# Kernel optimization log

Hardware: AMD Instinct MI355X
Metric: run time of the kernel (lower is better)

## Reference

```python
import jax, jax.numpy as jnp
import numpy as np

INPUT_DIM = 128
DEPTH = 6
HIDDEN = 64
NUM_INNER = 2 ** DEPTH - 1  # 63
NUM_LEAVES = 2 ** DEPTH     # 64


def setup_inputs() -> dict:
    key = jax.random.key(0)
    ks = jax.random.split(key, 6)
    x = jax.random.normal(ks[0], (65536, INPUT_DIM), dtype=jnp.float32)
    s1 = 1.0 / np.sqrt(INPUT_DIM)
    s2 = 1.0 / np.sqrt(HIDDEN)
    W1 = jax.random.uniform(ks[1], (NUM_INNER, INPUT_DIM, HIDDEN), minval=-s1, maxval=s1, dtype=jnp.float32)
    b1 = jax.random.uniform(ks[2], (NUM_INNER, HIDDEN), minval=-s1, maxval=s1, dtype=jnp.float32)
    W2 = jax.random.uniform(ks[3], (NUM_INNER, HIDDEN), minval=-s2, maxval=s2, dtype=jnp.float32)
    b2 = jax.random.uniform(ks[4], (NUM_INNER,), minval=-s2, maxval=s2, dtype=jnp.float32)
    leaf = jax.random.normal(ks[5], (NUM_LEAVES, 1), dtype=jnp.float32)
    return {"x": x, "W1": W1, "b1": b1, "W2": W2, "b2": b2, "leaf": leaf}


def reference(x, W1, b1, W2, b2, leaf):
    # All inner-node MLPs as one batched GEMM pair: [B, N] node probabilities
    h = jax.nn.relu(jnp.einsum('bi,nih->bnh', x, W1) + b1)      # [B, N, H]
    probs = jax.nn.sigmoid(jnp.einsum('bnh,nh->bn', h, W2) + b2)  # [B, N]

    # Original code walks node_idx = 2*node_idx+1 unconditionally, so the chain
    # of used node indices is 2^k - 1 for k = 0..depth-1.
    chain = jnp.array([2 ** k - 1 for k in range(DEPTH)], dtype=jnp.int32)
    p_chain = probs[:, chain]  # [B, D]

    # Bit k (LSB first) of leaf index selects p (bit=1) vs 1-p (bit=0)
    leaves = np.arange(NUM_LEAVES)
    bits = jnp.asarray(((leaves[:, None] >> np.arange(DEPTH)[None, :]) & 1).astype(np.float32))  # [L, D]

    # path_probs[b, l] = prod_k ( bits[l,k]*p + (1-bits[l,k])*(1-p) )
    factors = bits[None, :, :] * p_chain[:, None, :] + (1.0 - bits[None, :, :]) * (1.0 - p_chain[:, None, :])  # [B, L, D]
    path_probs = jnp.prod(factors, axis=-1)  # [B, L]

    return (path_probs @ leaf)[:, 0]  # [B]
```

## Files before the change

kernel.cpp:

```cpp
#include <hip/hip_runtime.h>

typedef __attribute__((ext_vector_type(4))) float f32x4;
typedef __attribute__((ext_vector_type(8))) short bf16x8;
typedef __attribute__((ext_vector_type(4))) unsigned int u32x4;

#define IDIM    128
#define HID     64
#define TDEPTH  6
#define MTILE   64
#define NWAVES  6
#define BLOCK   (NWAVES * 64)
#define T_TILES 4

__device__ __forceinline__ unsigned short f2bf(float f) {
    unsigned int u = __builtin_bit_cast(unsigned int, f);
    unsigned int r = (u + 0x7FFFu + ((u >> 16) & 1u)) >> 16;
    return (unsigned short)r;
}

__device__ __forceinline__ unsigned int f2bf_pk(float f0, float f1) {
    unsigned int u0 = __builtin_bit_cast(unsigned int, f0);
    unsigned int u1 = __builtin_bit_cast(unsigned int, f1);
    unsigned int t0 = u0 + 0x7FFFu + ((u0 >> 16) & 1u);
    unsigned int t1 = u1 + 0x7FFFu + ((u1 >> 16) & 1u);
    return (t1 & 0xFFFF0000u) | (t0 >> 16);
}

__global__ __launch_bounds__(BLOCK, 2)
void sdt_kernel(const float* __restrict__ x, const float* __restrict__ W1,
                const float* __restrict__ b1, const float* __restrict__ W2,
                const float* __restrict__ b2, const float* __restrict__ leaf,
                float* __restrict__ out) {
    __shared__ unsigned short xs[2][MTILE][IDIM + 8];
    __shared__ float p_lds[TDEPTH][MTILE];
    __shared__ float pp[4][MTILE];

    const int tid   = threadIdx.x;
    const int tile0 = blockIdx.x * T_TILES;

    const int wave = tid >> 6;
    const int lane = tid & 63;
    const int node = (1 << wave) - 1;
    const int lcol = lane & 15;
    const int lq   = lane >> 4;

    const float4* xv = reinterpret_cast<const float4*>(x);

    float4 sreg[6];
    {
        const float4* xt = xv + (size_t)tile0 * (MTILE * IDIM / 4);
        #pragma unroll
        for (int i = 0; i < 5; i++) sreg[i] = xt[tid + i * BLOCK];
        if (tid < 128) sreg[5] = xt[5 * BLOCK + tid];
    }

    bf16x8 bfrag[4][4];
    {
        const float* wsrc = W1 + (size_t)node * IDIM * HID + lcol;
        #pragma unroll
        for (int ks = 0; ks < 4; ks++) {
            const int k0 = ks * 32 + lq * 8;
            #pragma unroll
            for (int ct = 0; ct < 4; ct++) {
                const float* wc = wsrc + (size_t)k0 * HID + ct * 16;
                u32x4 pk;
                #pragma unroll
                for (int jp = 0; jp < 4; jp++)
                    pk[jp] = f2bf_pk(wc[(2 * jp) * HID], wc[(2 * jp + 1) * HID]);
                bfrag[ks][ct] = __builtin_bit_cast(bf16x8, pk);
            }
        }
    }

    float b1v[4], w2v[4];
    #pragma unroll
    for (int ct = 0; ct < 4; ct++) {
        int col = ct * 16 + lcol;
        b1v[ct] = b1[node * HID + col];
        w2v[ct] = W2[node * HID + col];
    }
    const float bias2 = b2[node];

    #pragma unroll
    for (int i = 0; i < 5; i++) {
        int f = tid + i * BLOCK, row = f >> 5, c4 = f & 31;
        float4 v = sreg[i];
        unsigned long long pk =
            (unsigned long long)f2bf(v.x) |
            ((unsigned long long)f2bf(v.y) << 16) |
            ((unsigned long long)f2bf(v.z) << 32) |
            ((unsigned long long)f2bf(v.w) << 48);
        *reinterpret_cast<unsigned long long*>(&xs[0][row][c4 * 4]) = pk;
    }
    if (tid < 128) {
        int f = 5 * BLOCK + tid, row = f >> 5, c4 = f & 31;
        float4 v = sreg[5];
        unsigned long long pk =
            (unsigned long long)f2bf(v.x) |
            ((unsigned long long)f2bf(v.y) << 16) |
            ((unsigned long long)f2bf(v.z) << 32) |
            ((unsigned long long)f2bf(v.w) << 48);
        *reinterpret_cast<unsigned long long*>(&xs[0][row][c4 * 4]) = pk;
    }
    __syncthreads();

    int cur = 0;
    for (int t = 0; t < T_TILES; ++t) {
        const bool pf = (t + 1 < T_TILES);
        if (pf) {
            const float4* xt = xv + (size_t)(tile0 + t + 1) * (MTILE * IDIM / 4);
            #pragma unroll
            for (int i = 0; i < 5; i++) sreg[i] = xt[tid + i * BLOCK];
            if (tid < 128) sreg[5] = xt[5 * BLOCK + tid];
        }

        f32x4 acc[4][4];
        #pragma unroll
        for (int rt = 0; rt < 4; rt++)
            #pragma unroll
            for (int ct = 0; ct < 4; ct++)
                acc[rt][ct] = (f32x4){0.f, 0.f, 0.f, 0.f};
        #pragma unroll
        for (int ks = 0; ks < 4; ks++) {
            bf16x8 afrag[4];
            #pragma unroll
            for (int rt = 0; rt < 4; rt++)
                afrag[rt] = *reinterpret_cast<const bf16x8*>(
                    &xs[cur][rt * 16 + lcol][ks * 32 + lq * 8]);
            #pragma unroll
            for (int rt = 0; rt < 4; rt++)
                #pragma unroll
                for (int ct = 0; ct < 4; ct++)
                    acc[rt][ct] = __builtin_amdgcn_mfma_f32_16x16x32_bf16(
                        afrag[rt], bfrag[ks][ct], acc[rt][ct], 0, 0, 0);
        }

        #pragma unroll
        for (int rt = 0; rt < 4; rt++) {
            #pragma unroll
            for (int r = 0; r < 4; r++) {
                float s = 0.f;
                #pragma unroll
                for (int ct = 0; ct < 4; ct++) {
                    float v = acc[rt][ct][r] + b1v[ct];
                    v = v > 0.f ? v : 0.f;
                    s += v * w2v[ct];
                }
                #pragma unroll
                for (int d = 1; d < 16; d <<= 1)
                    s += __shfl_xor(s, d, 64);
                float p = 1.f / (1.f + __expf(-(s + bias2)));
                if (lcol == 0)
                    p_lds[wave][rt * 16 + lq * 4 + r] = p;
            }
        }
        __syncthreads();

        if (pf) {
            #pragma unroll
            for (int i = 0; i < 5; i++) {
                int f = tid + i * BLOCK, row = f >> 5, c4 = f & 31;
                float4 v = sreg[i];
                unsigned long long pk =
                    (unsigned long long)f2bf(v.x) |
                    ((unsigned long long)f2bf(v.y) << 16) |
                    ((unsigned long long)f2bf(v.z) << 32) |
                    ((unsigned long long)f2bf(v.w) << 48);
                *reinterpret_cast<unsigned long long*>(&xs[cur ^ 1][row][c4 * 4]) = pk;
            }
            if (tid < 128) {
                int f = 5 * BLOCK + tid, row = f >> 5, c4 = f & 31;
                float4 v = sreg[5];
                unsigned long long pk =
                    (unsigned long long)f2bf(v.x) |
                    ((unsigned long long)f2bf(v.y) << 16) |
                    ((unsigned long long)f2bf(v.z) << 32) |
                    ((unsigned long long)f2bf(v.w) << 48);
                *reinterpret_cast<unsigned long long*>(&xs[cur ^ 1][row][c4 * 4]) = pk;
            }
        }

        if (tid < 4 * MTILE) {
            int row = tid & (MTILE - 1);
            int ch  = tid >> 6;
            float q0 = p_lds[0][row];
            float q1 = p_lds[1][row];
            float q2 = p_lds[2][row];
            float q3 = p_lds[3][row];
            float p4 = p_lds[4][row];
            float p5 = p_lds[5][row];
            float f4 = (ch & 1) ? p4 : 1.f - p4;
            float f5 = (ch & 2) ? p5 : 1.f - p5;
            const float* lf = leaf + ch * 16;
            float tt[8];
            #pragma unroll
            for (int j = 0; j < 8; j++) {
                float a = lf[2 * j], b = lf[2 * j + 1];
                tt[j] = a + q0 * (b - a);
            }
            #pragma unroll
            for (int j = 0; j < 4; j++) tt[j] = tt[2 * j] + q1 * (tt[2 * j + 1] - tt[2 * j]);
            #pragma unroll
            for (int j = 0; j < 2; j++) tt[j] = tt[2 * j] + q2 * (tt[2 * j + 1] - tt[2 * j]);
            float s = tt[0] + q3 * (tt[1] - tt[0]);
            pp[ch][row] = f4 * f5 * s;
        }
        __syncthreads();
        if (tid < MTILE)
            out[(size_t)(tile0 + t) * MTILE + tid] =
                (pp[0][tid] + pp[1][tid]) + (pp[2][tid] + pp[3][tid]);
        cur ^= 1;
    }
}

extern "C" void kernel_launch(void* const* d_in, const int* in_sizes, int n_in,
                              void* d_out, int out_size, void* d_ws, size_t ws_size,
                              hipStream_t stream) {
    const float* x    = (const float*)d_in[0];
    const float* W1   = (const float*)d_in[1];
    const float* b1   = (const float*)d_in[2];
    const float* W2   = (const float*)d_in[3];
    const float* b2   = (const float*)d_in[4];
    const float* leaf = (const float*)d_in[5];
    float* out = (float*)d_out;

    const int Bn = in_sizes[0] / IDIM;
    const int nblocks = Bn / (MTILE * T_TILES);

    (void)d_ws; (void)ws_size;
    sdt_kernel<<<nblocks, BLOCK, 0, stream>>>(x, W1, b1, W2, b2, leaf, out);
}
```

Measured before the change: 100.8 us.

## Drop register prefetch and double buffer, halve tiles per block, raise occupancy

Removes the register-staged prefetch of the next x tile and the double-buffered LDS tile, so the next tile is loaded synchronously into a single buffer after the current tile's MFMA work. It halves the tiles per block, which doubles the grid, and raises the launch-bounds occupancy target to 3 blocks per CU. It also caches leaf in LDS and defers the output write by one iteration using a double-buffered pp array. The aim is to cut register and LDS pressure so more waves hide memory latency, giving up the explicit in-block overlap of loads with compute.

```diff
diff --git a/kernel.cpp b/kernel.cpp
--- a/kernel.cpp
+++ b/kernel.cpp
@@ -10,7 +10,7 @@
 #define MTILE   64
 #define NWAVES  6
 #define BLOCK   (NWAVES * 64)
-#define T_TILES 4
+#define T_TILES 2
 
 __device__ __forceinline__ unsigned short f2bf(float f) {
     unsigned int u = __builtin_bit_cast(unsigned int, f);
@@ -26,14 +26,15 @@
     return (t1 & 0xFFFF0000u) | (t0 >> 16);
 }
 
-__global__ __launch_bounds__(BLOCK, 2)
+__global__ __launch_bounds__(BLOCK, 3)
 void sdt_kernel(const float* __restrict__ x, const float* __restrict__ W1,
                 const float* __restrict__ b1, const float* __restrict__ W2,
                 const float* __restrict__ b2, const float* __restrict__ leaf,
                 float* __restrict__ out) {
-    __shared__ unsigned short xs[2][MTILE][IDIM + 8];
+    __shared__ unsigned short xs[MTILE][IDIM + 8];
     __shared__ float p_lds[TDEPTH][MTILE];
-    __shared__ float pp[4][MTILE];
+    __shared__ float pp[2][4][MTILE];
+    __shared__ float leaf_lds[64];
 
     const int tid   = threadIdx.x;
     const int tile0 = blockIdx.x * T_TILES;
@@ -44,14 +45,22 @@
     const int lcol = lane & 15;
     const int lq   = lane >> 4;
 
+    if (tid < 64) leaf_lds[tid] = leaf[tid];
+
     const float4* xv = reinterpret_cast<const float4*>(x);
 
-    float4 sreg[6];
     {
         const float4* xt = xv + (size_t)tile0 * (MTILE * IDIM / 4);
-        #pragma unroll
-        for (int i = 0; i < 5; i++) sreg[i] = xt[tid + i * BLOCK];
-        if (tid < 128) sreg[5] = xt[5 * BLOCK + tid];
+        for (int f = tid; f < MTILE * (IDIM / 4); f += BLOCK) {
+            int row = f >> 5, c4 = f & 31;
+            float4 v = xt[f];
+            unsigned long long pk =
+                (unsigned long long)f2bf(v.x) |
+                ((unsigned long long)f2bf(v.y) << 16) |
+                ((unsigned long long)f2bf(v.z) << 32) |
+                ((unsigned long long)f2bf(v.w) << 48);
+            *reinterpret_cast<unsigned long long*>(&xs[row][c4 * 4]) = pk;
+        }
     }
 
     bf16x8 bfrag[4][4];
@@ -81,39 +90,9 @@
     }
     const float bias2 = b2[node];
 
-    #pragma unroll
-    for (int i = 0; i < 5; i++) {
-        int f = tid + i * BLOCK, row = f >> 5, c4 = f & 31;
-        float4 v = sreg[i];
-        unsigned long long pk =
-            (unsigned long long)f2bf(v.x) |
-            ((unsigned long long)f2bf(v.y) << 16) |
-            ((unsigned long long)f2bf(v.z) << 32) |
-            ((unsigned long long)f2bf(v.w) << 48);
-        *reinterpret_cast<unsigned long long*>(&xs[0][row][c4 * 4]) = pk;
-    }
-    if (tid < 128) {
-        int f = 5 * BLOCK + tid, row = f >> 5, c4 = f & 31;
-        float4 v = sreg[5];
-        unsigned long long pk =
-            (unsigned long long)f2bf(v.x) |
-            ((unsigned long long)f2bf(v.y) << 16) |
-            ((unsigned long long)f2bf(v.z) << 32) |
-            ((unsigned long long)f2bf(v.w) << 48);
-        *reinterpret_cast<unsigned long long*>(&xs[0][row][c4 * 4]) = pk;
-    }
     __syncthreads();
 
-    int cur = 0;
     for (int t = 0; t < T_TILES; ++t) {
-        const bool pf = (t + 1 < T_TILES);
-        if (pf) {
-            const float4* xt = xv + (size_t)(tile0 + t + 1) * (MTILE * IDIM / 4);
-            #pragma unroll
-            for (int i = 0; i < 5; i++) sreg[i] = xt[tid + i * BLOCK];
-            if (tid < 128) sreg[5] = xt[5 * BLOCK + tid];
-        }
-
         f32x4 acc[4][4];
         #pragma unroll
         for (int rt = 0; rt < 4; rt++)
@@ -122,17 +101,15 @@
                 acc[rt][ct] = (f32x4){0.f, 0.f, 0.f, 0.f};
         #pragma unroll
         for (int ks = 0; ks < 4; ks++) {
-            bf16x8 afrag[4];
-            #pragma unroll
-            for (int rt = 0; rt < 4; rt++)
-                afrag[rt] = *reinterpret_cast<const bf16x8*>(
-                    &xs[cur][rt * 16 + lcol][ks * 32 + lq * 8]);
-            #pragma unroll
-            for (int rt = 0; rt < 4; rt++)
+            #pragma unroll
+            for (int rt = 0; rt < 4; rt++) {
+                bf16x8 afrag = *reinterpret_cast<const bf16x8*>(
+                    &xs[rt * 16 + lcol][ks * 32 + lq * 8]);
                 #pragma unroll
                 for (int ct = 0; ct < 4; ct++)
                     acc[rt][ct] = __builtin_amdgcn_mfma_f32_16x16x32_bf16(
-                        afrag[rt], bfrag[ks][ct], acc[rt][ct], 0, 0, 0);
+                        afrag, bfrag[ks][ct], acc[rt][ct], 0, 0, 0);
+            }
         }
 
         #pragma unroll
@@ -156,28 +133,11 @@
         }
         __syncthreads();
 
-        if (pf) {
-            #pragma unroll
-            for (int i = 0; i < 5; i++) {
-                int f = tid + i * BLOCK, row = f >> 5, c4 = f & 31;
-                float4 v = sreg[i];
-                unsigned long long pk =
-                    (unsigned long long)f2bf(v.x) |
-                    ((unsigned long long)f2bf(v.y) << 16) |
-                    ((unsigned long long)f2bf(v.z) << 32) |
-                    ((unsigned long long)f2bf(v.w) << 48);
-                *reinterpret_cast<unsigned long long*>(&xs[cur ^ 1][row][c4 * 4]) = pk;
-            }
-            if (tid < 128) {
-                int f = 5 * BLOCK + tid, row = f >> 5, c4 = f & 31;
-                float4 v = sreg[5];
-                unsigned long long pk =
-                    (unsigned long long)f2bf(v.x) |
-                    ((unsigned long long)f2bf(v.y) << 16) |
-                    ((unsigned long long)f2bf(v.z) << 32) |
-                    ((unsigned long long)f2bf(v.w) << 48);
-                *reinterpret_cast<unsigned long long*>(&xs[cur ^ 1][row][c4 * 4]) = pk;
-            }
+        if (t > 0 && tid < MTILE) {
+            const float* q = &pp[(t - 1) & 1][0][0];
+            out[(size_t)(tile0 + t - 1) * MTILE + tid] =
+                (q[0 * MTILE + tid] + q[1 * MTILE + tid]) +
+                (q[2 * MTILE + tid] + q[3 * MTILE + tid]);
         }
 
         if (tid < 4 * MTILE) {
@@ -191,7 +151,7 @@
             float p5 = p_lds[5][row];
             float f4 = (ch & 1) ? p4 : 1.f - p4;
             float f5 = (ch & 2) ? p5 : 1.f - p5;
-            const float* lf = leaf + ch * 16;
+            const float* lf = leaf_lds + ch * 16;
             float tt[8];
             #pragma unroll
             for (int j = 0; j < 8; j++) {
@@ -203,13 +163,30 @@
             #pragma unroll
             for (int j = 0; j < 2; j++) tt[j] = tt[2 * j] + q2 * (tt[2 * j + 1] - tt[2 * j]);
             float s = tt[0] + q3 * (tt[1] - tt[0]);
-            pp[ch][row] = f4 * f5 * s;
+            pp[t & 1][ch][row] = f4 * f5 * s;
+        }
+
+        if (t + 1 < T_TILES) {
+            const float4* xt = xv + (size_t)(tile0 + t + 1) * (MTILE * IDIM / 4);
+            for (int f = tid; f < MTILE * (IDIM / 4); f += BLOCK) {
+                int row = f >> 5, c4 = f & 31;
+                float4 v = xt[f];
+                unsigned long long pk =
+                    (unsigned long long)f2bf(v.x) |
+                    ((unsigned long long)f2bf(v.y) << 16) |
+                    ((unsigned long long)f2bf(v.z) << 32) |
+                    ((unsigned long long)f2bf(v.w) << 48);
+                *reinterpret_cast<unsigned long long*>(&xs[row][c4 * 4]) = pk;
+            }
         }
         __syncthreads();
-        if (tid < MTILE)
-            out[(size_t)(tile0 + t) * MTILE + tid] =
-                (pp[0][tid] + pp[1][tid]) + (pp[2][tid] + pp[3][tid]);
-        cur ^= 1;
+    }
+
+    if (tid < MTILE) {
+        const float* q = &pp[(T_TILES - 1) & 1][0][0];
+        out[(size_t)(tile0 + T_TILES - 1) * MTILE + tid] =
+            (q[0 * MTILE + tid] + q[1 * MTILE + tid]) +
+            (q[2 * MTILE + tid] + q[3 * MTILE + tid]);
     }
 }
 
```

Result: slower. 113.9 us (+13.0%).
